# Kernel tuning notes

Hardware: AMD Instinct MI355X
Metric: run time of the kernel (lower is better)

The kernel has to match this reference:

```python
import jax, jax.numpy as jnp
import numpy as np

N_NODES = 50000
N_EDGES = 800000
EPS = 1e-12


def _l2norm(x):
    # F.normalize(x, p=2, dim=1)
    n = jnp.sqrt(jnp.sum(x * x, axis=1, keepdims=True))
    return x / jnp.maximum(n, EPS)


def _sage_layer(h, src, dst, inv_deg, W_self, W_neigh, b, last):
    # mean aggregation over in-neighbors: gather src feats, scatter-add to dst
    msg = jax.ops.segment_sum(h[src], dst, num_segments=N_NODES)  # [N, d]
    h_neigh = msg * inv_deg  # [N, d]
    rst = h @ W_self + h_neigh @ W_neigh + b
    if not last:
        rst = jax.nn.relu(rst)
        rst = _l2norm(rst)
    return rst


def setup_inputs() -> dict:
    key = jax.random.key(0)
    ks = jax.random.split(key, 10)
    d_in, d_h, d_out = 128, 128, 64
    s = lambda k, sh, fan: jax.random.normal(k, sh, jnp.float32) / np.sqrt(fan)
    return {
        "features": jax.random.normal(ks[0], (N_NODES, d_in), jnp.float32),
        "src": jax.random.randint(ks[1], (N_EDGES,), 0, N_NODES, jnp.int32),
        "dst": jax.random.randint(ks[2], (N_EDGES,), 0, N_NODES, jnp.int32),
        "W_self0": s(ks[3], (d_in, d_h), d_in),
        "W_neigh0": s(ks[4], (d_in, d_h), d_in),
        "b0": jnp.zeros((d_h,), jnp.float32),
        "W_self1": s(ks[5], (d_h, d_h), d_h),
        "W_neigh1": s(ks[6], (d_h, d_h), d_h),
        "b1": jnp.zeros((d_h,), jnp.float32),
        "W_self2": s(ks[7], (d_h, d_out), d_h),
        "W_neigh2": s(ks[8], (d_h, d_out), d_h),
        "b2": jnp.zeros((d_out,), jnp.float32),
    }


def reference(features, src, dst, W_self0, W_neigh0, b0, W_self1, W_neigh1, b1, W_self2, W_neigh2, b2):
    # in-degree for mean aggregation (clamped to avoid div-by-zero)
    deg = jax.ops.segment_sum(jnp.ones((N_EDGES,), jnp.float32), dst, num_segments=N_NODES)
    inv_deg = (1.0 / jnp.maximum(deg, 1.0))[:, None]  # [N,1]
    h = _sage_layer(features, src, dst, inv_deg, W_self0, W_neigh0, b0, last=False)
    h = _sage_layer(h, src, dst, inv_deg, W_self1, W_neigh1, b1, last=False)
    out = _sage_layer(h, src, dst, inv_deg, W_self2, W_neigh2, b2, last=True)
    return out
```

## Files before the change

### kernel.cpp

```cpp
#include <hip/hip_runtime.h>
#include <hip/hip_bf16.h>

#define N_NODES 50000
#define N_EDGES 800000
#define NBUCKET 196
#define NPB 256
#define BUCKET_CAP 7168
#define BUCKET_PAD 8192
#define PART_EDGES 4096
#define PART_BLOCKS ((N_EDGES + PART_EDGES - 1) / PART_EDGES)
#define SENTINEL 0xFFFFFFFFu

typedef __attribute__((ext_vector_type(8))) short bf16x8;
typedef __attribute__((ext_vector_type(4))) float f32x4;

__device__ __forceinline__ float bf2f(unsigned short u) {
    unsigned int x = ((unsigned int)u) << 16;
    return __uint_as_float(x);
}
__device__ __forceinline__ unsigned short f2bf(float f) {
    unsigned int x = __float_as_uint(f);
    unsigned int lsb = (x >> 16) & 1u;
    x += 0x7fffu + lsb;
    return (unsigned short)(x >> 16);
}

#define NF2 ((N_NODES * 64 + 255) / 256)
__global__ __launch_bounds__(256) void k_prep(
        const float* __restrict__ Ws0, const float* __restrict__ Wn0,
        const float* __restrict__ Ws1, const float* __restrict__ Wn1,
        const float* __restrict__ Ws2, const float* __restrict__ Wn2,
        __hip_bfloat16* __restrict__ frag0, __hip_bfloat16* __restrict__ frag1,
        __hip_bfloat16* __restrict__ frag2,
        const float2* __restrict__ fin, unsigned int* __restrict__ fout,
        unsigned int* __restrict__ z1, unsigned int* __restrict__ z2,
        int* __restrict__ cursor, int* __restrict__ valid) {
    int b = blockIdx.x;
    if (b >= 40 + NF2) {
        int tid = threadIdx.x;
        if (tid < NBUCKET) { cursor[tid] = 0; valid[tid] = 0; }
        if (tid < 64)       fout[(size_t)N_NODES * 64 + tid] = 0;
        else if (tid < 128) z1[(size_t)N_NODES * 64 + (tid - 64)] = 0;
        else if (tid < 192) z2[(size_t)N_NODES * 64 + (tid - 128)] = 0;
        return;
    }
    if (b >= 40) {
        int i = (b - 40) * 256 + threadIdx.x;
        if (i < N_NODES * 64) {
            float2 v = fin[i];
            fout[i] = ((unsigned int)f2bf(v.y) << 16) | (unsigned int)f2bf(v.x);
        }
        return;
    }
    const float* Wself;
    const float* Wneigh;
    __hip_bfloat16* frag;
    int Dout, lb;
    if (b < 16)      { Wself = Ws0; Wneigh = Wn0; frag = frag0; Dout = 128; lb = b; }
    else if (b < 32) { Wself = Ws1; Wneigh = Wn1; frag = frag1; Dout = 128; lb = b - 16; }
    else             { Wself = Ws2; Wneigh = Wn2; frag = frag2; Dout = 64;  lb = b - 32; }
    int t = lb * 256 + threadIdx.x;
    int nCt = Dout >> 4;
    int total = nCt * 8 * 64;
    if (t >= total) return;
    int lane = t & 63;
    int kt = (t >> 6) & 7;
    int ct = t >> 9;
    int q = lane >> 4;
    int n = ct * 16 + (lane & 15);
    unsigned short* dstp = (unsigned short*)frag + ((size_t)((ct * 8 + kt) * 64 + lane)) * 8;
    #pragma unroll
    for (int j = 0; j < 8; ++j) {
        int k = kt * 32 + q * 8 + j;
        float v = (k < 128) ? Wself[k * Dout + n] : Wneigh[(k - 128) * Dout + n];
        dstp[j] = f2bf(v);
    }
}

__global__ __launch_bounds__(256) void k_partA(const int* __restrict__ src,
                                               const int* __restrict__ dst,
                                               int* __restrict__ cursor,
                                               int* __restrict__ valid,
                                               unsigned int* __restrict__ bucketArr) {
    __shared__ int hist[NBUCKET];
    __shared__ int base[NBUCKET];
    __shared__ int cnt[NBUCKET];
    int tid = threadIdx.x;
    if (tid < NBUCKET) hist[tid] = 0;
    __syncthreads();
    int e0 = blockIdx.x * PART_EDGES;
    for (int j = 0; j < PART_EDGES; j += 256) {
        int e = e0 + j + tid;
        if (e < N_EDGES) atomicAdd(&hist[dst[e] >> 8], 1);
    }
    __syncthreads();
    if (tid < NBUCKET) {
        int h = hist[tid];
        int hp = (h + 15) & ~15;
        int b0 = atomicAdd(&cursor[tid], hp);
        atomicAdd(&valid[tid], h);
        base[tid] = b0;
        cnt[tid] = 0;
        for (int k = h; k < hp; ++k) {
            int p = b0 + k;
            if (p < BUCKET_CAP) bucketArr[(size_t)tid * BUCKET_CAP + p] = SENTINEL;
        }
    }
    __syncthreads();
    for (int j = 0; j < PART_EDGES; j += 256) {
        int e = e0 + j + tid;
        if (e < N_EDGES) {
            int d = dst[e];
            int b = d >> 8;
            int p = base[b] + atomicAdd(&cnt[b], 1);
            if (p < BUCKET_CAP)
                bucketArr[(size_t)b * BUCKET_CAP + p] =
                    (unsigned int)src[e] | ((unsigned int)(d & 255) << 16);
        }
    }
}

__global__ __launch_bounds__(256) void k_partB(const unsigned int* __restrict__ bucketArr,
                                               const int* __restrict__ cursor,
                                               int* __restrict__ off_beg,
                                               int* __restrict__ off_end,
                                               float* __restrict__ inv_deg,
                                               int* __restrict__ edge_src) {
    __shared__ unsigned int ed[BUCKET_CAP];
    __shared__ int csr[BUCKET_CAP];
    __shared__ int hist[256];
    __shared__ int lbase[256];
    __shared__ int lcnt[256];
    __shared__ int tot_s;
    int b = blockIdx.x;
    int tid = threadIdx.x;
    int size = min(cursor[b], BUCKET_CAP);
    int B0 = b * BUCKET_PAD;
    int nbase = b * NPB;
    int ncount = min(NPB, N_NODES - nbase);
    hist[tid] = 0;
    __syncthreads();
    for (int j = 0; j < BUCKET_CAP; j += 256) {
        int i = j + tid;
        if (i < size) {
            unsigned int u = bucketArr[(size_t)b * BUCKET_CAP + i];
            ed[i] = u;
            if ((u >> 16) < 256u) atomicAdd(&hist[u >> 16], 1);
        }
    }
    __syncthreads();
    int v = hist[tid];
    int pv = (v + 15) & ~15;
    lbase[tid] = pv;
    __syncthreads();
    for (int off = 1; off < 256; off <<= 1) {
        int t = (tid >= off) ? lbase[tid - off] : 0;
        __syncthreads();
        lbase[tid] += t;
        __syncthreads();
    }
    int excl = lbase[tid] - pv;
    if (tid == 255) tot_s = lbase[255];
    __syncthreads();
    lbase[tid] = excl;
    lcnt[tid] = 0;
    if (tid < ncount) {
        off_beg[nbase + tid] = B0 + excl;
        off_end[nbase + tid] = B0 + excl + pv;
        inv_deg[nbase + tid] = 1.0f / (float)max(v, 1);
    }
    __syncthreads();
    int tot = min(tot_s, BUCKET_CAP);
    for (int j = tid; j < tot; j += 256) csr[j] = N_NODES;
    __syncthreads();
    for (int j = 0; j < BUCKET_CAP; j += 256) {
        int i = j + tid;
        if (i < size) {
            unsigned int u = ed[i];
            unsigned int ld = u >> 16;
            if (ld < 256u) {
                int p = lbase[ld] + atomicAdd(&lcnt[ld], 1);
                if (p < BUCKET_CAP) csr[p] = (int)(u & 0xffffu) + nbase - nbase + (int)(u & 0xffffu) * 0;
            }
        }
    }
    __syncthreads();
    for (int j = tid; j < tot; j += 256) edge_src[B0 + j] = csr[j];
}

__global__ void k_agg(const __hip_bfloat16* __restrict__ hv,
                      const int* __restrict__ off_beg, const int* __restrict__ off_end,
                      const int* __restrict__ edge_src, const float* __restrict__ inv_deg,
                      __hip_bfloat16* __restrict__ msg) {
    int gid = blockIdx.x * blockDim.x + threadIdx.x;
    int node = gid >> 6;
    int lane = gid & 63;
    if (node >= N_NODES) return;
    int quad = lane >> 4;
    int sub = lane & 15;
    int beg = off_beg[node], endp = off_end[node];
    const uint4* hp = (const uint4*)hv;

    float a0[8], a1[8], a2[8], a3[8];
    #pragma unroll
    for (int c = 0; c < 8; ++c) { a0[c] = 0.f; a1[c] = 0.f; a2[c] = 0.f; a3[c] = 0.f; }

    for (int i = beg; i < endp; i += 16) {
        int s0 = edge_src[i + quad];
        int s1 = edge_src[i + 4 + quad];
        int s2 = edge_src[i + 8 + quad];
        int s3 = edge_src[i + 12 + quad];
        uint4 u0 = hp[(size_t)s0 * 16 + sub];
        uint4 u1 = hp[(size_t)s1 * 16 + sub];
        uint4 u2 = hp[(size_t)s2 * 16 + sub];
        uint4 u3 = hp[(size_t)s3 * 16 + sub];
        a0[0] += bf2f((unsigned short)(u0.x & 0xffffu)); a0[1] += bf2f((unsigned short)(u0.x >> 16));
        a0[2] += bf2f((unsigned short)(u0.y & 0xffffu)); a0[3] += bf2f((unsigned short)(u0.y >> 16));
        a0[4] += bf2f((unsigned short)(u0.z & 0xffffu)); a0[5] += bf2f((unsigned short)(u0.z >> 16));
        a0[6] += bf2f((unsigned short)(u0.w & 0xffffu)); a0[7] += bf2f((unsigned short)(u0.w >> 16));
        a1[0] += bf2f((unsigned short)(u1.x & 0xffffu)); a1[1] += bf2f((unsigned short)(u1.x >> 16));
        a1[2] += bf2f((unsigned short)(u1.y & 0xffffu)); a1[3] += bf2f((unsigned short)(u1.y >> 16));
        a1[4] += bf2f((unsigned short)(u1.z & 0xffffu)); a1[5] += bf2f((unsigned short)(u1.z >> 16));
        a1[6] += bf2f((unsigned short)(u1.w & 0xffffu)); a1[7] += bf2f((unsigned short)(u1.w >> 16));
        a2[0] += bf2f((unsigned short)(u2.x & 0xffffu)); a2[1] += bf2f((unsigned short)(u2.x >> 16));
        a2[2] += bf2f((unsigned short)(u2.y & 0xffffu)); a2[3] += bf2f((unsigned short)(u2.y >> 16));
        a2[4] += bf2f((unsigned short)(u2.z & 0xffffu)); a2[5] += bf2f((unsigned short)(u2.z >> 16));
        a2[6] += bf2f((unsigned short)(u2.w & 0xffffu)); a2[7] += bf2f((unsigned short)(u2.w >> 16));
        a3[0] += bf2f((unsigned short)(u3.x & 0xffffu)); a3[1] += bf2f((unsigned short)(u3.x >> 16));
        a3[2] += bf2f((unsigned short)(u3.y & 0xffffu)); a3[3] += bf2f((unsigned short)(u3.y >> 16));
        a3[4] += bf2f((unsigned short)(u3.z & 0xffffu)); a3[5] += bf2f((unsigned short)(u3.z >> 16));
        a3[6] += bf2f((unsigned short)(u3.w & 0xffffu)); a3[7] += bf2f((unsigned short)(u3.w >> 16));
    }

    float r[8];
    #pragma unroll
    for (int c = 0; c < 8; ++c) {
        float t = a0[c] + a1[c] + a2[c] + a3[c];
        t += __shfl_xor(t, 16);
        t += __shfl_xor(t, 32);
        r[c] = t;
    }
    if (quad == 0) {
        float w = inv_deg[node];
        uint4 o;
        o.x = ((unsigned int)f2bf(r[1] * w) << 16) | (unsigned int)f2bf(r[0] * w);
        o.y = ((unsigned int)f2bf(r[3] * w) << 16) | (unsigned int)f2bf(r[2] * w);
        o.z = ((unsigned int)f2bf(r[5] * w) << 16) | (unsigned int)f2bf(r[4] * w);
        o.w = ((unsigned int)f2bf(r[7] * w) << 16) | (unsigned int)f2bf(r[6] * w);
        ((uint4*)msg)[(size_t)node * 16 + sub] = o;
    }
}

template <int NCT, bool LAST>
__global__ __launch_bounds__(256) void k_gemm(const __hip_bfloat16* __restrict__ Aself,
                                              const __hip_bfloat16* __restrict__ Aneigh,
                                              const __hip_bfloat16* __restrict__ frag,
                                              const float* __restrict__ bias,
                                              void* __restrict__ out_) {
    constexpr int Dout = NCT * 16;
    int tid = threadIdx.x;
    int wv = tid >> 6, lane = tid & 63;
    int n0 = blockIdx.x * 64 + wv * 16;
    if (n0 >= N_NODES) return;
    int q = lane >> 4, l15 = lane & 15;
    int rowA = n0 + l15;
    if (rowA > N_NODES - 1) rowA = N_NODES - 1;

    f32x4 acc[NCT];
    #pragma unroll
    for (int c = 0; c < NCT; ++c) acc[c] = (f32x4){0.f, 0.f, 0.f, 0.f};

    const bf16x8* fragv = (const bf16x8*)frag;
    #pragma unroll
    for (int kt = 0; kt < 8; ++kt) {
        int kb = (kt & 3) * 32 + q * 8;
        const __hip_bfloat16* Ab = (kt < 4) ? Aself : Aneigh;
        bf16x8 a = *(const bf16x8*)(Ab + (size_t)rowA * 128 + kb);
        #pragma unroll
        for (int ct = 0; ct < NCT; ++ct) {
            bf16x8 b = fragv[(ct * 8 + kt) * 64 + lane];
            acc[ct] = __builtin_amdgcn_mfma_f32_16x16x32_bf16(a, b, acc[ct], 0, 0, 0);
        }
    }

    float ss[4] = {0.f, 0.f, 0.f, 0.f};
    #pragma unroll
    for (int ct = 0; ct < NCT; ++ct) {
        float bc = bias[ct * 16 + l15];
        #pragma unroll
        for (int r = 0; r < 4; ++r) {
            float v = acc[ct][r] + bc;
            if (!LAST) v = fmaxf(v, 0.0f);
            acc[ct][r] = v;
            ss[r] += v * v;
        }
    }

    float scale[4];
    #pragma unroll
    for (int r = 0; r < 4; ++r) {
        if (!LAST) {
            float s = ss[r];
            s += __shfl_xor(s, 1);
            s += __shfl_xor(s, 2);
            s += __shfl_xor(s, 4);
            s += __shfl_xor(s, 8);
            scale[r] = 1.0f / fmaxf(sqrtf(s), 1e-12f);
        } else {
            scale[r] = 1.0f;
        }
    }

    #pragma unroll
    for (int ct = 0; ct < NCT; ++ct) {
        #pragma unroll
        for (int r = 0; r < 4; ++r) {
            int row = n0 + q * 4 + r;
            if (row < N_NODES) {
                float v = acc[ct][r] * scale[r];
                if (LAST)
                    ((float*)out_)[(size_t)row * Dout + ct * 16 + l15] = v;
                else
                    ((unsigned short*)out_)[(size_t)row * Dout + ct * 16 + l15] = f2bf(v);
            }
        }
    }
}


extern "C" void kernel_launch(void* const* d_in, const int* in_sizes, int n_in,
                              void* d_out, int out_size, void* d_ws, size_t ws_size,
                              hipStream_t stream) {
    const float* features = (const float*)d_in[0];
    const int* src = (const int*)d_in[1];
    const int* dst = (const int*)d_in[2];
    const float* Ws0 = (const float*)d_in[3];
    const float* Wn0 = (const float*)d_in[4];
    const float* b0  = (const float*)d_in[5];
    const float* Ws1 = (const float*)d_in[6];
    const float* Wn1 = (const float*)d_in[7];
    const float* b1  = (const float*)d_in[8];
    const float* Ws2 = (const float*)d_in[9];
    const float* Wn2 = (const float*)d_in[10];
    const float* b2  = (const float*)d_in[11];
    float* out = (float*)d_out;

    char* ws = (char*)d_ws;
    size_t off = 0;
    auto alloc = [&](size_t bytes) -> void* {
        void* p = ws + off;
        off = (off + bytes + 255) & ~(size_t)255;
        return p;
    };
    int*   cursor   = (int*)alloc((size_t)NBUCKET * 4);
    int*   valid    = (int*)alloc((size_t)NBUCKET * 4);
    unsigned int* bucketArr = (unsigned int*)alloc((size_t)NBUCKET * BUCKET_CAP * 4);
    int*   off_beg  = (int*)alloc((size_t)N_NODES * 4);
    int*   off_end  = (int*)alloc((size_t)N_NODES * 4);
    int*   edge_src = (int*)alloc((size_t)NBUCKET * BUCKET_PAD * 4);
    float* inv_deg  = (float*)alloc((size_t)N_NODES * 4);
    __hip_bfloat16* fbf = (__hip_bfloat16*)alloc((size_t)(N_NODES + 1) * 128 * 2);
    __hip_bfloat16* msg = (__hip_bfloat16*)alloc((size_t)N_NODES * 128 * 2);
    __hip_bfloat16* h1  = (__hip_bfloat16*)alloc((size_t)(N_NODES + 1) * 128 * 2);
    __hip_bfloat16* h2  = (__hip_bfloat16*)alloc((size_t)(N_NODES + 1) * 128 * 2);
    __hip_bfloat16* frag0 = (__hip_bfloat16*)alloc((size_t)8 * 8 * 64 * 8 * 2);
    __hip_bfloat16* frag1 = (__hip_bfloat16*)alloc((size_t)8 * 8 * 64 * 8 * 2);
    __hip_bfloat16* frag2 = (__hip_bfloat16*)alloc((size_t)4 * 8 * 64 * 8 * 2);

    k_prep<<<40 + NF2 + 1, 256, 0, stream>>>(Ws0, Wn0, Ws1, Wn1, Ws2, Wn2,
                                             frag0, frag1, frag2,
                                             (const float2*)features, (unsigned int*)fbf,
                                             (unsigned int*)h1, (unsigned int*)h2,
                                             cursor, valid);
    k_partA<<<PART_BLOCKS, 256, 0, stream>>>(src, dst, cursor, valid, bucketArr);
    k_partB<<<NBUCKET, 256, 0, stream>>>(bucketArr, cursor,
                                         off_beg, off_end, inv_deg, edge_src);

    const int aggGrid = (N_NODES * 64) / 256;
    const int gemmGrid = (N_NODES + 63) / 64;

    k_agg<<<aggGrid, 256, 0, stream>>>(fbf, off_beg, off_end, edge_src, inv_deg, msg);
    k_gemm<8, false><<<gemmGrid, 256, 0, stream>>>(fbf, msg, frag0, b0, h1);
    k_agg<<<aggGrid, 256, 0, stream>>>(h1, off_beg, off_end, edge_src, inv_deg, msg);
    k_gemm<8, false><<<gemmGrid, 256, 0, stream>>>(h1, msg, frag1, b1, h2);
    k_agg<<<aggGrid, 256, 0, stream>>>(h2, off_beg, off_end, edge_src, inv_deg, msg);
    k_gemm<4, true><<<gemmGrid, 256, 0, stream>>>(h2, msg, frag2, b2, out);
}
```

Before: 266.4 us.

## Split aggregation across four column slices with more edges per wavefront

The neighbor aggregation kernel now splits each node's 128 feature columns into four slices, each handled by a separate block, so every wavefront processes 16 edges in parallel with four lanes per edge, covering 32 edges per iteration. This is meant to raise memory-level parallelism and cut wasted iterations on the padded edge lists for low-degree nodes. It adds a tail iteration and extra shuffle reductions, and loads edge indices and stores messages with nontemporal hints. Each edge index is now read four times, once per slice, and the launch has four times as many blocks.

```diff
diff --git a/kernel.cpp b/kernel.cpp
--- a/kernel.cpp
+++ b/kernel.cpp
@@ -13,6 +13,7 @@
 
 typedef __attribute__((ext_vector_type(8))) short bf16x8;
 typedef __attribute__((ext_vector_type(4))) float f32x4;
+typedef __attribute__((ext_vector_type(4))) unsigned int u32x4;
 
 __device__ __forceinline__ float bf2f(unsigned short u) {
     unsigned int x = ((unsigned int)u) << 16;
@@ -180,7 +181,7 @@
             unsigned int ld = u >> 16;
             if (ld < 256u) {
                 int p = lbase[ld] + atomicAdd(&lcnt[ld], 1);
-                if (p < BUCKET_CAP) csr[p] = (int)(u & 0xffffu) + nbase - nbase + (int)(u & 0xffffu) * 0;
+                if (p < BUCKET_CAP) csr[p] = (int)(u & 0xffffu);
             }
         }
     }
@@ -188,32 +189,31 @@
     for (int j = tid; j < tot; j += 256) edge_src[B0 + j] = csr[j];
 }
 
+#define NSLICE 4
 __global__ void k_agg(const __hip_bfloat16* __restrict__ hv,
                       const int* __restrict__ off_beg, const int* __restrict__ off_end,
                       const int* __restrict__ edge_src, const float* __restrict__ inv_deg,
                       __hip_bfloat16* __restrict__ msg) {
-    int gid = blockIdx.x * blockDim.x + threadIdx.x;
-    int node = gid >> 6;
-    int lane = gid & 63;
+    int slice = blockIdx.x & (NSLICE - 1);
+    int node = (blockIdx.x >> 2) * 4 + (threadIdx.x >> 6);
     if (node >= N_NODES) return;
-    int quad = lane >> 4;
-    int sub = lane & 15;
+    int lane = threadIdx.x & 63;
+    int e4 = lane >> 2;
+    int part = lane & 3;
     int beg = off_beg[node], endp = off_end[node];
-    const uint4* hp = (const uint4*)hv;
-
-    float a0[8], a1[8], a2[8], a3[8];
-    #pragma unroll
-    for (int c = 0; c < 8; ++c) { a0[c] = 0.f; a1[c] = 0.f; a2[c] = 0.f; a3[c] = 0.f; }
-
-    for (int i = beg; i < endp; i += 16) {
-        int s0 = edge_src[i + quad];
-        int s1 = edge_src[i + 4 + quad];
-        int s2 = edge_src[i + 8 + quad];
-        int s3 = edge_src[i + 12 + quad];
-        uint4 u0 = hp[(size_t)s0 * 16 + sub];
-        uint4 u1 = hp[(size_t)s1 * 16 + sub];
-        uint4 u2 = hp[(size_t)s2 * 16 + sub];
-        uint4 u3 = hp[(size_t)s3 * 16 + sub];
+    const u32x4* hp = (const u32x4*)hv;
+    int colbase = slice * 4 + part;
+
+    float a0[8], a1[8];
+    #pragma unroll
+    for (int c = 0; c < 8; ++c) { a0[c] = 0.f; a1[c] = 0.f; }
+
+    int i = beg;
+    for (; i + 32 <= endp; i += 32) {
+        int s0 = __builtin_nontemporal_load(edge_src + i + e4);
+        int s1 = __builtin_nontemporal_load(edge_src + i + 16 + e4);
+        u32x4 u0 = hp[(size_t)s0 * 16 + colbase];
+        u32x4 u1 = hp[(size_t)s1 * 16 + colbase];
         a0[0] += bf2f((unsigned short)(u0.x & 0xffffu)); a0[1] += bf2f((unsigned short)(u0.x >> 16));
         a0[2] += bf2f((unsigned short)(u0.y & 0xffffu)); a0[3] += bf2f((unsigned short)(u0.y >> 16));
         a0[4] += bf2f((unsigned short)(u0.z & 0xffffu)); a0[5] += bf2f((unsigned short)(u0.z >> 16));
@@ -222,32 +222,34 @@
         a1[2] += bf2f((unsigned short)(u1.y & 0xffffu)); a1[3] += bf2f((unsigned short)(u1.y >> 16));
         a1[4] += bf2f((unsigned short)(u1.z & 0xffffu)); a1[5] += bf2f((unsigned short)(u1.z >> 16));
         a1[6] += bf2f((unsigned short)(u1.w & 0xffffu)); a1[7] += bf2f((unsigned short)(u1.w >> 16));
-        a2[0] += bf2f((unsigned short)(u2.x & 0xffffu)); a2[1] += bf2f((unsigned short)(u2.x >> 16));
-        a2[2] += bf2f((unsigned short)(u2.y & 0xffffu)); a2[3] += bf2f((unsigned short)(u2.y >> 16));
-        a2[4] += bf2f((unsigned short)(u2.z & 0xffffu)); a2[5] += bf2f((unsigned short)(u2.z >> 16));
-        a2[6] += bf2f((unsigned short)(u2.w & 0xffffu)); a2[7] += bf2f((unsigned short)(u2.w >> 16));
-        a3[0] += bf2f((unsigned short)(u3.x & 0xffffu)); a3[1] += bf2f((unsigned short)(u3.x >> 16));
-        a3[2] += bf2f((unsigned short)(u3.y & 0xffffu)); a3[3] += bf2f((unsigned short)(u3.y >> 16));
-        a3[4] += bf2f((unsigned short)(u3.z & 0xffffu)); a3[5] += bf2f((unsigned short)(u3.z >> 16));
-        a3[6] += bf2f((unsigned short)(u3.w & 0xffffu)); a3[7] += bf2f((unsigned short)(u3.w >> 16));
+    }
+    if (i < endp) {
+        int s0 = __builtin_nontemporal_load(edge_src + i + e4);
+        u32x4 u0 = hp[(size_t)s0 * 16 + colbase];
+        a0[0] += bf2f((unsigned short)(u0.x & 0xffffu)); a0[1] += bf2f((unsigned short)(u0.x >> 16));
+        a0[2] += bf2f((unsigned short)(u0.y & 0xffffu)); a0[3] += bf2f((unsigned short)(u0.y >> 16));
+        a0[4] += bf2f((unsigned short)(u0.z & 0xffffu)); a0[5] += bf2f((unsigned short)(u0.z >> 16));
+        a0[6] += bf2f((unsigned short)(u0.w & 0xffffu)); a0[7] += bf2f((unsigned short)(u0.w >> 16));
     }
 
     float r[8];
     #pragma unroll
     for (int c = 0; c < 8; ++c) {
-        float t = a0[c] + a1[c] + a2[c] + a3[c];
+        float t = a0[c] + a1[c];
+        t += __shfl_xor(t, 4);
+        t += __shfl_xor(t, 8);
         t += __shfl_xor(t, 16);
         t += __shfl_xor(t, 32);
         r[c] = t;
     }
-    if (quad == 0) {
+    if (e4 == 0) {
         float w = inv_deg[node];
-        uint4 o;
+        u32x4 o;
         o.x = ((unsigned int)f2bf(r[1] * w) << 16) | (unsigned int)f2bf(r[0] * w);
         o.y = ((unsigned int)f2bf(r[3] * w) << 16) | (unsigned int)f2bf(r[2] * w);
         o.z = ((unsigned int)f2bf(r[5] * w) << 16) | (unsigned int)f2bf(r[4] * w);
         o.w = ((unsigned int)f2bf(r[7] * w) << 16) | (unsigned int)f2bf(r[6] * w);
-        ((uint4*)msg)[(size_t)node * 16 + sub] = o;
+        __builtin_nontemporal_store(o, (u32x4*)msg + (size_t)node * 16 + colbase);
     }
 }
 
@@ -376,7 +378,7 @@
     k_partB<<<NBUCKET, 256, 0, stream>>>(bucketArr, cursor,
                                          off_beg, off_end, inv_deg, edge_src);
 
-    const int aggGrid = (N_NODES * 64) / 256;
+    const int aggGrid = NSLICE * ((N_NODES + 3) / 4);
     const int gemmGrid = (N_NODES + 63) / 64;
 
     k_agg<<<aggGrid, 256, 0, stream>>>(fbf, off_beg, off_end, edge_src, inv_deg, msg);
```

Result: slower. 400.0 us (+50.2%).

## Fuse neighbor aggregation and GEMM into one kernel per SAGE layer

Applied to the files above, without the earlier changes.

Merges the per-layer aggregation and GEMM kernels into a single 1024-thread kernel. Each block aggregates 16 nodes into LDS, then splits the output columns across waves for MFMA, with a cross-wave LDS reduction for the L2 norm. This drops the global msg buffer round trip and three kernel launches. The cost is that GEMM waves run only one column tile each, half the waves sit idle in the last layer, and the large block size may limit occupancy for the gather phase.

```diff
diff --git a/kernel.cpp b/kernel.cpp
--- a/kernel.cpp
+++ b/kernel.cpp
@@ -10,6 +10,7 @@
 #define PART_EDGES 4096
 #define PART_BLOCKS ((N_EDGES + PART_EDGES - 1) / PART_EDGES)
 #define SENTINEL 0xFFFFFFFFu
+#define LDS_ROW 136
 
 typedef __attribute__((ext_vector_type(8))) short bf16x8;
 typedef __attribute__((ext_vector_type(4))) float f32x4;
@@ -180,7 +181,7 @@
             unsigned int ld = u >> 16;
             if (ld < 256u) {
                 int p = lbase[ld] + atomicAdd(&lcnt[ld], 1);
-                if (p < BUCKET_CAP) csr[p] = (int)(u & 0xffffu) + nbase - nbase + (int)(u & 0xffffu) * 0;
+                if (p < BUCKET_CAP) csr[p] = (int)(u & 0xffffu);
             }
         }
     }
@@ -188,141 +189,129 @@
     for (int j = tid; j < tot; j += 256) edge_src[B0 + j] = csr[j];
 }
 
-__global__ void k_agg(const __hip_bfloat16* __restrict__ hv,
-                      const int* __restrict__ off_beg, const int* __restrict__ off_end,
-                      const int* __restrict__ edge_src, const float* __restrict__ inv_deg,
-                      __hip_bfloat16* __restrict__ msg) {
-    int gid = blockIdx.x * blockDim.x + threadIdx.x;
-    int node = gid >> 6;
-    int lane = gid & 63;
-    if (node >= N_NODES) return;
-    int quad = lane >> 4;
-    int sub = lane & 15;
-    int beg = off_beg[node], endp = off_end[node];
-    const uint4* hp = (const uint4*)hv;
-
-    float a0[8], a1[8], a2[8], a3[8];
-    #pragma unroll
-    for (int c = 0; c < 8; ++c) { a0[c] = 0.f; a1[c] = 0.f; a2[c] = 0.f; a3[c] = 0.f; }
-
-    for (int i = beg; i < endp; i += 16) {
-        int s0 = edge_src[i + quad];
-        int s1 = edge_src[i + 4 + quad];
-        int s2 = edge_src[i + 8 + quad];
-        int s3 = edge_src[i + 12 + quad];
-        uint4 u0 = hp[(size_t)s0 * 16 + sub];
-        uint4 u1 = hp[(size_t)s1 * 16 + sub];
-        uint4 u2 = hp[(size_t)s2 * 16 + sub];
-        uint4 u3 = hp[(size_t)s3 * 16 + sub];
-        a0[0] += bf2f((unsigned short)(u0.x & 0xffffu)); a0[1] += bf2f((unsigned short)(u0.x >> 16));
-        a0[2] += bf2f((unsigned short)(u0.y & 0xffffu)); a0[3] += bf2f((unsigned short)(u0.y >> 16));
-        a0[4] += bf2f((unsigned short)(u0.z & 0xffffu)); a0[5] += bf2f((unsigned short)(u0.z >> 16));
-        a0[6] += bf2f((unsigned short)(u0.w & 0xffffu)); a0[7] += bf2f((unsigned short)(u0.w >> 16));
-        a1[0] += bf2f((unsigned short)(u1.x & 0xffffu)); a1[1] += bf2f((unsigned short)(u1.x >> 16));
-        a1[2] += bf2f((unsigned short)(u1.y & 0xffffu)); a1[3] += bf2f((unsigned short)(u1.y >> 16));
-        a1[4] += bf2f((unsigned short)(u1.z & 0xffffu)); a1[5] += bf2f((unsigned short)(u1.z >> 16));
-        a1[6] += bf2f((unsigned short)(u1.w & 0xffffu)); a1[7] += bf2f((unsigned short)(u1.w >> 16));
-        a2[0] += bf2f((unsigned short)(u2.x & 0xffffu)); a2[1] += bf2f((unsigned short)(u2.x >> 16));
-        a2[2] += bf2f((unsigned short)(u2.y & 0xffffu)); a2[3] += bf2f((unsigned short)(u2.y >> 16));
-        a2[4] += bf2f((unsigned short)(u2.z & 0xffffu)); a2[5] += bf2f((unsigned short)(u2.z >> 16));
-        a2[6] += bf2f((unsigned short)(u2.w & 0xffffu)); a2[7] += bf2f((unsigned short)(u2.w >> 16));
-        a3[0] += bf2f((unsigned short)(u3.x & 0xffffu)); a3[1] += bf2f((unsigned short)(u3.x >> 16));
-        a3[2] += bf2f((unsigned short)(u3.y & 0xffffu)); a3[3] += bf2f((unsigned short)(u3.y >> 16));
-        a3[4] += bf2f((unsigned short)(u3.z & 0xffffu)); a3[5] += bf2f((unsigned short)(u3.z >> 16));
-        a3[6] += bf2f((unsigned short)(u3.w & 0xffffu)); a3[7] += bf2f((unsigned short)(u3.w >> 16));
-    }
-
-    float r[8];
-    #pragma unroll
-    for (int c = 0; c < 8; ++c) {
-        float t = a0[c] + a1[c] + a2[c] + a3[c];
-        t += __shfl_xor(t, 16);
-        t += __shfl_xor(t, 32);
-        r[c] = t;
-    }
-    if (quad == 0) {
-        float w = inv_deg[node];
-        uint4 o;
-        o.x = ((unsigned int)f2bf(r[1] * w) << 16) | (unsigned int)f2bf(r[0] * w);
-        o.y = ((unsigned int)f2bf(r[3] * w) << 16) | (unsigned int)f2bf(r[2] * w);
-        o.z = ((unsigned int)f2bf(r[5] * w) << 16) | (unsigned int)f2bf(r[4] * w);
-        o.w = ((unsigned int)f2bf(r[7] * w) << 16) | (unsigned int)f2bf(r[6] * w);
-        ((uint4*)msg)[(size_t)node * 16 + sub] = o;
-    }
-}
-
 template <int NCT, bool LAST>
-__global__ __launch_bounds__(256) void k_gemm(const __hip_bfloat16* __restrict__ Aself,
-                                              const __hip_bfloat16* __restrict__ Aneigh,
-                                              const __hip_bfloat16* __restrict__ frag,
-                                              const float* __restrict__ bias,
-                                              void* __restrict__ out_) {
+__global__ __launch_bounds__(1024) void k_fused(
+        const __hip_bfloat16* __restrict__ hv,
+        const int* __restrict__ off_beg, const int* __restrict__ off_end,
+        const int* __restrict__ edge_src, const float* __restrict__ inv_deg,
+        const __hip_bfloat16* __restrict__ frag,
+        const float* __restrict__ bias,
+        void* __restrict__ out_) {
+    __shared__ __hip_bfloat16 mean[16 * LDS_ROW];
+    __shared__ float ssp[8][16];
     constexpr int Dout = NCT * 16;
     int tid = threadIdx.x;
-    int wv = tid >> 6, lane = tid & 63;
-    int n0 = blockIdx.x * 64 + wv * 16;
-    if (n0 >= N_NODES) return;
+    int w = tid >> 6;
+    int lane = tid & 63;
+    int nbase = blockIdx.x * 16;
+    int node = nbase + w;
+
+    {
+        int quad = lane >> 4;
+        int sub = lane & 15;
+        int beg = off_beg[node], endp = off_end[node];
+        const uint4* hp = (const uint4*)hv;
+        float a0[8], a1[8], a2[8], a3[8];
+        #pragma unroll
+        for (int c = 0; c < 8; ++c) { a0[c] = 0.f; a1[c] = 0.f; a2[c] = 0.f; a3[c] = 0.f; }
+        for (int i = beg; i < endp; i += 16) {
+            int s0 = edge_src[i + quad];
+            int s1 = edge_src[i + 4 + quad];
+            int s2 = edge_src[i + 8 + quad];
+            int s3 = edge_src[i + 12 + quad];
+            uint4 u0 = hp[(size_t)s0 * 16 + sub];
+            uint4 u1 = hp[(size_t)s1 * 16 + sub];
+            uint4 u2 = hp[(size_t)s2 * 16 + sub];
+            uint4 u3 = hp[(size_t)s3 * 16 + sub];
+            a0[0] += bf2f((unsigned short)(u0.x & 0xffffu)); a0[1] += bf2f((unsigned short)(u0.x >> 16));
+            a0[2] += bf2f((unsigned short)(u0.y & 0xffffu)); a0[3] += bf2f((unsigned short)(u0.y >> 16));
+            a0[4] += bf2f((unsigned short)(u0.z & 0xffffu)); a0[5] += bf2f((unsigned short)(u0.z >> 16));
+            a0[6] += bf2f((unsigned short)(u0.w & 0xffffu)); a0[7] += bf2f((unsigned short)(u0.w >> 16));
+            a1[0] += bf2f((unsigned short)(u1.x & 0xffffu)); a1[1] += bf2f((unsigned short)(u1.x >> 16));
+            a1[2] += bf2f((unsigned short)(u1.y & 0xffffu)); a1[3] += bf2f((unsigned short)(u1.y >> 16));
+            a1[4] += bf2f((unsigned short)(u1.z & 0xffffu)); a1[5] += bf2f((unsigned short)(u1.z >> 16));
+            a1[6] += bf2f((unsigned short)(u1.w & 0xffffu)); a1[7] += bf2f((unsigned short)(u1.w >> 16));
+            a2[0] += bf2f((unsigned short)(u2.x & 0xffffu)); a2[1] += bf2f((unsigned short)(u2.x >> 16));
+            a2[2] += bf2f((unsigned short)(u2.y & 0xffffu)); a2[3] += bf2f((unsigned short)(u2.y >> 16));
+            a2[4] += bf2f((unsigned short)(u2.z & 0xffffu)); a2[5] += bf2f((unsigned short)(u2.z >> 16));
+            a2[6] += bf2f((unsigned short)(u2.w & 0xffffu)); a2[7] += bf2f((unsigned short)(u2.w >> 16));
+            a3[0] += bf2f((unsigned short)(u3.x & 0xffffu)); a3[1] += bf2f((unsigned short)(u3.x >> 16));
+            a3[2] += bf2f((unsigned short)(u3.y & 0xffffu)); a3[3] += bf2f((unsigned short)(u3.y >> 16));
+            a3[4] += bf2f((unsigned short)(u3.z & 0xffffu)); a3[5] += bf2f((unsigned short)(u3.z >> 16));
+            a3[6] += bf2f((unsigned short)(u3.w & 0xffffu)); a3[7] += bf2f((unsigned short)(u3.w >> 16));
+        }
+        float r[8];
+        #pragma unroll
+        for (int c = 0; c < 8; ++c) {
+            float t = a0[c] + a1[c] + a2[c] + a3[c];
+            t += __shfl_xor(t, 16);
+            t += __shfl_xor(t, 32);
+            r[c] = t;
+        }
+        if (quad == 0) {
+            float wgt = inv_deg[node];
+            uint4 o;
+            o.x = ((unsigned int)f2bf(r[1] * wgt) << 16) | (unsigned int)f2bf(r[0] * wgt);
+            o.y = ((unsigned int)f2bf(r[3] * wgt) << 16) | (unsigned int)f2bf(r[2] * wgt);
+            o.z = ((unsigned int)f2bf(r[5] * wgt) << 16) | (unsigned int)f2bf(r[4] * wgt);
+            o.w = ((unsigned int)f2bf(r[7] * wgt) << 16) | (unsigned int)f2bf(r[6] * wgt);
+            *(uint4*)((char*)mean + (size_t)w * (LDS_ROW * 2) + sub * 16) = o;
+        }
+    }
+    __syncthreads();
+
+    bool active = (w < NCT);
     int q = lane >> 4, l15 = lane & 15;
-    int rowA = n0 + l15;
-    if (rowA > N_NODES - 1) rowA = N_NODES - 1;
-
-    f32x4 acc[NCT];
-    #pragma unroll
-    for (int c = 0; c < NCT; ++c) acc[c] = (f32x4){0.f, 0.f, 0.f, 0.f};
-
-    const bf16x8* fragv = (const bf16x8*)frag;
-    #pragma unroll
-    for (int kt = 0; kt < 8; ++kt) {
-        int kb = (kt & 3) * 32 + q * 8;
-        const __hip_bfloat16* Ab = (kt < 4) ? Aself : Aneigh;
-        bf16x8 a = *(const bf16x8*)(Ab + (size_t)rowA * 128 + kb);
-        #pragma unroll
-        for (int ct = 0; ct < NCT; ++ct) {
-            bf16x8 b = fragv[(ct * 8 + kt) * 64 + lane];
-            acc[ct] = __builtin_amdgcn_mfma_f32_16x16x32_bf16(a, b, acc[ct], 0, 0, 0);
-        }
-    }
-
-    float ss[4] = {0.f, 0.f, 0.f, 0.f};
-    #pragma unroll
-    for (int ct = 0; ct < NCT; ++ct) {
-        float bc = bias[ct * 16 + l15];
+    f32x4 acc = (f32x4){0.f, 0.f, 0.f, 0.f};
+    if (active) {
+        int rowA = nbase + l15;
+        const bf16x8* fragv = (const bf16x8*)frag;
+        #pragma unroll
+        for (int kt = 0; kt < 8; ++kt) {
+            int kb = (kt & 3) * 32 + q * 8;
+            bf16x8 a;
+            if (kt < 4) a = *(const bf16x8*)(hv + (size_t)rowA * 128 + kb);
+            else        a = *(const bf16x8*)((const char*)mean + (size_t)l15 * (LDS_ROW * 2) + kb * 2);
+            bf16x8 b = fragv[(w * 8 + kt) * 64 + lane];
+            acc = __builtin_amdgcn_mfma_f32_16x16x32_bf16(a, b, acc, 0, 0, 0);
+        }
+        float bc = bias[w * 16 + l15];
         #pragma unroll
         for (int r = 0; r < 4; ++r) {
-            float v = acc[ct][r] + bc;
+            float v = acc[r] + bc;
             if (!LAST) v = fmaxf(v, 0.0f);
-            acc[ct][r] = v;
-            ss[r] += v * v;
-        }
-    }
-
-    float scale[4];
-    #pragma unroll
-    for (int r = 0; r < 4; ++r) {
+            acc[r] = v;
+        }
         if (!LAST) {
-            float s = ss[r];
-            s += __shfl_xor(s, 1);
-            s += __shfl_xor(s, 2);
-            s += __shfl_xor(s, 4);
-            s += __shfl_xor(s, 8);
-            scale[r] = 1.0f / fmaxf(sqrtf(s), 1e-12f);
-        } else {
-            scale[r] = 1.0f;
-        }
-    }
-
-    #pragma unroll
-    for (int ct = 0; ct < NCT; ++ct) {
+            #pragma unroll
+            for (int r = 0; r < 4; ++r) {
+                float s = acc[r] * acc[r];
+                s += __shfl_xor(s, 1);
+                s += __shfl_xor(s, 2);
+                s += __shfl_xor(s, 4);
+                s += __shfl_xor(s, 8);
+                if (l15 == 0) ssp[w][q * 4 + r] = s;
+            }
+        }
+    }
+    __syncthreads();
+    if (active) {
         #pragma unroll
         for (int r = 0; r < 4; ++r) {
-            int row = n0 + q * 4 + r;
-            if (row < N_NODES) {
-                float v = acc[ct][r] * scale[r];
-                if (LAST)
-                    ((float*)out_)[(size_t)row * Dout + ct * 16 + l15] = v;
-                else
-                    ((unsigned short*)out_)[(size_t)row * Dout + ct * 16 + l15] = f2bf(v);
+            float scale = 1.0f;
+            if (!LAST) {
+                int row = q * 4 + r;
+                float s = 0.f;
+                #pragma unroll
+                for (int w2 = 0; w2 < NCT; ++w2) s += ssp[w2][row];
+                scale = 1.0f / fmaxf(sqrtf(s), 1e-12f);
             }
+            int grow = nbase + q * 4 + r;
+            float v = acc[r] * scale;
+            if (LAST)
+                ((float*)out_)[(size_t)grow * Dout + w * 16 + l15] = v;
+            else
+                ((unsigned short*)out_)[(size_t)grow * 128 + w * 16 + l15] = f2bf(v);
         }
     }
 }
@@ -360,7 +349,6 @@
     int*   edge_src = (int*)alloc((size_t)NBUCKET * BUCKET_PAD * 4);
     float* inv_deg  = (float*)alloc((size_t)N_NODES * 4);
     __hip_bfloat16* fbf = (__hip_bfloat16*)alloc((size_t)(N_NODES + 1) * 128 * 2);
-    __hip_bfloat16* msg = (__hip_bfloat16*)alloc((size_t)N_NODES * 128 * 2);
     __hip_bfloat16* h1  = (__hip_bfloat16*)alloc((size_t)(N_NODES + 1) * 128 * 2);
     __hip_bfloat16* h2  = (__hip_bfloat16*)alloc((size_t)(N_NODES + 1) * 128 * 2);
     __hip_bfloat16* frag0 = (__hip_bfloat16*)alloc((size_t)8 * 8 * 64 * 8 * 2);
@@ -376,13 +364,9 @@
     k_partB<<<NBUCKET, 256, 0, stream>>>(bucketArr, cursor,
                                          off_beg, off_end, inv_deg, edge_src);
 
-    const int aggGrid = (N_NODES * 64) / 256;
-    const int gemmGrid = (N_NODES + 63) / 64;
-
-    k_agg<<<aggGrid, 256, 0, stream>>>(fbf, off_beg, off_end, edge_src, inv_deg, msg);
-    k_gemm<8, false><<<gemmGrid, 256, 0, stream>>>(fbf, msg, frag0, b0, h1);
-    k_agg<<<aggGrid, 256, 0, stream>>>(h1, off_beg, off_end, edge_src, inv_deg, msg);
-    k_gemm<8, false><<<gemmGrid, 256, 0, stream>>>(h1, msg, frag1, b1, h2);
-    k_agg<<<aggGrid, 256, 0, stream>>>(h2, off_beg, off_end, edge_src, inv_deg, msg);
-    k_gemm<4, true><<<gemmGrid, 256, 0, stream>>>(h2, msg, frag2, b2, out);
-}
+    const int fusedGrid = N_NODES / 16;
+
+    k_fused<8, false><<<fusedGrid, 1024, 0, stream>>>(fbf, off_beg, off_end, edge_src, inv_deg, frag0, b0, h1);
+    k_fused<8, false><<<fusedGrid, 1024, 0, stream>>>(h1, off_beg, off_end, edge_src, inv_deg, frag1, b1, h2);
+    k_fused<4, true><<<fusedGrid, 1024, 0, stream>>>(h2, off_beg, off_end, edge_src, inv_deg, frag2, b2, out);
+}
```

Measured after the change: 332.3 us. +24.7%, slower.
